# Performance work log

Hardware: AMD Instinct MI355X
Metric: run time of the kernel (lower is better)

Reference implementation:

```python
import jax, jax.numpy as jnp
import numpy as np


def _reduce1(x):
    # x: [B, n, d] -> [B, 2d]; exists=max, forall=min over objects (exclude_self is a no-op for cnt=1)
    return jnp.concatenate([x.max(axis=1), x.min(axis=1)], axis=-1)


def _reduce2(x):
    # x: [B, n, n, d] -> [B, n, 2d]; exclude_self masks diagonal i==j (0 for exists/max, 1 for forall/min)
    n = x.shape[1]
    diag = jnp.eye(n, dtype=bool)[None, :, :, None]
    exists = jnp.where(diag, 0.0, x).max(axis=2)
    forall = jnp.where(diag, 1.0, x).min(axis=2)
    return jnp.concatenate([exists, forall], axis=-1)


def _layer(f0, f1, f2, p):
    # One LogicLayer step (breadth=2, minmax reducer, exclude_self, sigmoid norm, no hidden layers)
    W0, b0, W1, b1, W2, b2 = p
    B, n, d1 = f1.shape
    # order 0: [self, reduce(order1)]
    g0 = jnp.concatenate([f0, _reduce1(f1)], axis=-1)
    o0 = jax.nn.sigmoid(g0 @ W0 + b0)
    # order 1: [expand(order0), self, reduce(order2)]
    e0 = jnp.broadcast_to(f0[:, None, :], (B, n, f0.shape[-1]))
    g1 = jnp.concatenate([e0, f1, _reduce2(f2)], axis=-1)
    o1 = jax.nn.sigmoid(g1 @ W1 + b1)
    # order 2: [expand(order1), self] then Permutation(2) = cat(x, swap(i,j))
    e1 = jnp.broadcast_to(f1[:, :, None, :], (B, n, n, d1))
    g2 = jnp.concatenate([e1, f2], axis=-1)
    g2 = jnp.concatenate([g2, jnp.swapaxes(g2, 1, 2)], axis=-1)
    o2 = jax.nn.sigmoid(g2 @ W2 + b2)
    return o0, o1, o2


def setup_inputs() -> dict:
    key = jax.random.key(0)
    B, n = 4, 256
    d = [32, 64, 64]
    O = 128
    ks = iter(jax.random.split(key, 64))
    inp = {
        "x0": jax.random.uniform(next(ks), (B, d[0]), dtype=jnp.float32),
        "x1": jax.random.uniform(next(ks), (B, n, d[1]), dtype=jnp.float32),
        "x2": jax.random.uniform(next(ks), (B, n, n, d[2]), dtype=jnp.float32),
    }
    fan_ins = [
        (d[0] + 2 * d[1], d[0] + d[1] + 2 * d[2], 2 * (d[1] + d[2])),  # layer 0
        (O + 2 * O, O + O + 2 * O, 2 * (O + O)),                        # layer 1
        (O + 2 * O, O + O + 2 * O, 2 * (O + O)),                        # layer 2
    ]
    for l, fins in enumerate(fan_ins):
        for o, fin in enumerate(fins):
            inp[f"W{o}_{l}"] = jax.random.normal(next(ks), (fin, O), dtype=jnp.float32) / np.sqrt(fin).astype(np.float32)
            inp[f"b{o}_{l}"] = jnp.zeros((O,), dtype=jnp.float32)
    return inp


def reference(x0, x1, x2,
              W0_0, b0_0, W1_0, b1_0, W2_0, b2_0,
              W0_1, b0_1, W1_1, b1_1, W2_1, b2_1,
              W0_2, b0_2, W1_2, b1_2, W2_2, b2_2):
    f = (x0, x1, x2)
    for p in ((W0_0, b0_0, W1_0, b1_0, W2_0, b2_0),
              (W0_1, b0_1, W1_1, b1_1, W2_1, b2_1),
              (W0_2, b0_2, W1_2, b1_2, W2_2, b2_2)):
        f = _layer(*f, p)
    return f
```

## Files before the change

### kernel.cpp

```cpp
#include <hip/hip_runtime.h>
#include <hip/hip_bf16.h>
#include <cstdint>

#define NN 256
#define NB 4
#define OC 128

using bf16x8_t = __attribute__((ext_vector_type(8))) __bf16;
using f32x4_t  = __attribute__((ext_vector_type(4))) float;

typedef const __attribute__((address_space(1))) uint8_t* gptr1_t;
typedef __attribute__((address_space(3))) uint8_t* lptr3_t;

__device__ __forceinline__ void async_load16(const void* g, void* l) {
  __builtin_amdgcn_global_load_lds((gptr1_t)g, (lptr3_t)l, 16, 0, 0);
}

__device__ __forceinline__ float sigf(float x) {
  return 1.0f / (1.0f + __expf(-x));
}

__device__ __forceinline__ uint16_t f2bf_rne(float f) {
  uint32_t u = __float_as_uint(f);
  uint32_t r = (u + 0x7fffu + ((u >> 16) & 1u)) >> 16;
  return (uint16_t)r;
}

__device__ __forceinline__ void emit_wt(const float* __restrict__ W2,
                                        uint16_t* __restrict__ Wt, int d1,
                                        int d2, int idx) {
  const int K = 2 * d2;
  const int nn = idx / K, k = idx - nn * K;
  const int row = (k < d2) ? (d1 + k) : (2 * d1 + d2 + (k - d2));
  Wt[idx] = f2bf_rne(W2[row * OC + nn]);
}

__device__ __forceinline__ void emit_bt(const float* __restrict__ W1,
                                        const float* __restrict__ W2, uint16_t* __restrict__ Bt,
                                        int D0, int D1, int D2, int FIN1,
                                        int KP, int idx) {
  const int n = idx / KP, k = idx - n * KP;
  float val = 0.f;
  if (n < 128) {
    if (k < FIN1) val = W1[k * OC + n];
  } else if (n < 256) {
    if (k >= D0 && k < D0 + D1) val = W2[(k - D0) * OC + (n - 128)];
  } else {
    if (k >= D0 && k < D0 + D1) val = W2[(D1 + D2 + (k - D0)) * OC + (n - 256)];
  }
  Bt[idx] = f2bf_rne(val);
}

__global__ __launch_bounds__(256) void prep_all(
    const float* __restrict__ W2_0, const float* __restrict__ W2_1,
    const float* __restrict__ W2_2, const float* __restrict__ W1_0,
    const float* __restrict__ W1_1, const float* __restrict__ W1_2,
    const float* __restrict__ x0, const float* __restrict__ x1,
    uint16_t* __restrict__ Wt0, uint16_t* __restrict__ Wt1,
    uint16_t* __restrict__ Wt2, uint16_t* __restrict__ Bt0,
    uint16_t* __restrict__ Bt1, uint16_t* __restrict__ Bt2,
    uint16_t* __restrict__ g1bf0, float* __restrict__ r2b,
    float* __restrict__ r2c, unsigned* __restrict__ cnt) {
  int g = blockIdx.x * 256 + threadIdx.x;
  if (g < 16384) { emit_wt(W2_0, Wt0, 64, 64, g); return; }
  g -= 16384;
  if (g < 32768) { emit_wt(W2_1, Wt1, 128, 128, g); return; }
  g -= 32768;
  if (g < 32768) { emit_wt(W2_2, Wt2, 128, 128, g); return; }
  g -= 32768;
  if (g < 98304) { emit_bt(W1_0, W2_0, Bt0, 32, 64, 64, 224, 256, g); return; }
  g -= 98304;
  if (g < 196608) { emit_bt(W1_1, W2_1, Bt1, 128, 128, 128, 512, 512, g); return; }
  g -= 196608;
  if (g < 196608) { emit_bt(W1_2, W2_2, Bt2, 128, 128, 128, 512, 512, g); return; }
  g -= 196608;
  if (g < 131072) {
    const int row = g >> 7, t = g & 127;
    uint16_t* const gp = g1bf0 + (size_t)row * 256;
    if (t < 32) gp[t] = f2bf_rne(x0[(row >> 8) * 32 + t]);
    else if (t < 96) gp[t] = f2bf_rne(x1[(size_t)row * 64 + (t - 32)]);
    else gp[128 + t] = 0;
    return;
  }
  g -= 131072;
  if (g < 262144) { r2b[g] = ((g & 255) < 128) ? 0.f : 1.f; return; }
  g -= 262144;
  if (g < 262144) { r2c[g] = ((g & 255) < 128) ? 0.f : 1.f; return; }
  g -= 262144;
  if (g < 2048) cnt[g] = 0u;
}

__global__ __launch_bounds__(256) void reduce2_l0_kernel(
    const float* __restrict__ x2, uint16_t* __restrict__ g1bf0,
    uint16_t* __restrict__ x2bf) {
  const int bid = blockIdx.x;
  const int i = bid & 255;
  const int tid = threadIdx.x;
  const int q = tid & 15, s = tid >> 4;
  const size_t rowbase = ((size_t)bid * NN) * 64 + q * 4;
  float mxA0 = 0.f, mxA1 = 0.f, mxA2 = 0.f, mxA3 = 0.f;
  float mnA0 = 1.f, mnA1 = 1.f, mnA2 = 1.f, mnA3 = 1.f;
  float mxB0 = 0.f, mxB1 = 0.f, mxB2 = 0.f, mxB3 = 0.f;
  float mnB0 = 1.f, mnB1 = 1.f, mnB2 = 1.f, mnB3 = 1.f;
#pragma unroll 2
  for (int t = 0; t < 16; t += 2) {
    const int jA = s + t * 16, jB = jA + 16;
    const float4 xa = *(const float4*)(x2 + rowbase + (size_t)jA * 64);
    const float4 xb = *(const float4*)(x2 + rowbase + (size_t)jB * 64);
    uint2 pa, pb;
    pa.x = (uint32_t)f2bf_rne(xa.x) | ((uint32_t)f2bf_rne(xa.y) << 16);
    pa.y = (uint32_t)f2bf_rne(xa.z) | ((uint32_t)f2bf_rne(xa.w) << 16);
    pb.x = (uint32_t)f2bf_rne(xb.x) | ((uint32_t)f2bf_rne(xb.y) << 16);
    pb.y = (uint32_t)f2bf_rne(xb.z) | ((uint32_t)f2bf_rne(xb.w) << 16);
    *(uint2*)(x2bf + rowbase + (size_t)jA * 64) = pa;
    *(uint2*)(x2bf + rowbase + (size_t)jB * 64) = pb;
    if (jA != i) {
      mxA0 = fmaxf(mxA0, xa.x); mxA1 = fmaxf(mxA1, xa.y);
      mxA2 = fmaxf(mxA2, xa.z); mxA3 = fmaxf(mxA3, xa.w);
      mnA0 = fminf(mnA0, xa.x); mnA1 = fminf(mnA1, xa.y);
      mnA2 = fminf(mnA2, xa.z); mnA3 = fminf(mnA3, xa.w);
    }
    if (jB != i) {
      mxB0 = fmaxf(mxB0, xb.x); mxB1 = fmaxf(mxB1, xb.y);
      mxB2 = fmaxf(mxB2, xb.z); mxB3 = fmaxf(mxB3, xb.w);
      mnB0 = fminf(mnB0, xb.x); mnB1 = fminf(mnB1, xb.y);
      mnB2 = fminf(mnB2, xb.z); mnB3 = fminf(mnB3, xb.w);
    }
  }
  float mx0 = fmaxf(mxA0, mxB0), mx1 = fmaxf(mxA1, mxB1);
  float mx2 = fmaxf(mxA2, mxB2), mx3 = fmaxf(mxA3, mxB3);
  float mn0 = fminf(mnA0, mnB0), mn1 = fminf(mnA1, mnB1);
  float mn2 = fminf(mnA2, mnB2), mn3 = fminf(mnA3, mnB3);
  __shared__ float4 smx[256], smn[256];
  smx[tid] = make_float4(mx0, mx1, mx2, mx3);
  smn[tid] = make_float4(mn0, mn1, mn2, mn3);
  __syncthreads();
  if (s == 0) {
    for (int ss = 1; ss < 16; ++ss) {
      float4 a = smx[q + ss * 16], c = smn[q + ss * 16];
      mx0 = fmaxf(mx0, a.x); mx1 = fmaxf(mx1, a.y);
      mx2 = fmaxf(mx2, a.z); mx3 = fmaxf(mx3, a.w);
      mn0 = fminf(mn0, c.x); mn1 = fminf(mn1, c.y);
      mn2 = fminf(mn2, c.z); mn3 = fminf(mn3, c.w);
    }
    uint16_t* const g = g1bf0 + (size_t)bid * 256;
    g[96 + q * 4 + 0] = f2bf_rne(mx0); g[96 + q * 4 + 1] = f2bf_rne(mx1);
    g[96 + q * 4 + 2] = f2bf_rne(mx2); g[96 + q * 4 + 3] = f2bf_rne(mx3);
    g[160 + q * 4 + 0] = f2bf_rne(mn0); g[160 + q * 4 + 1] = f2bf_rne(mn1);
    g[160 + q * 4 + 2] = f2bf_rne(mn2); g[160 + q * 4 + 3] = f2bf_rne(mn3);
  }
}

template <int KP, int D0, int D1, bool DUP>
__global__ __launch_bounds__(256) void small_gemm(
    const uint16_t* __restrict__ g1, const uint16_t* __restrict__ Bt,
    const float* __restrict__ b1, const float* __restrict__ b2,
    float* __restrict__ f1out, uint16_t* __restrict__ g1next,
    float* __restrict__ u, float* __restrict__ v,
    const float* __restrict__ f0in, const float* __restrict__ f1in,
    const float* __restrict__ W0, const float* __restrict__ b0,
    float* __restrict__ f0out) {
  constexpr int NCH = KP / 64;
  const int bid = blockIdx.x;
  const int tid = threadIdx.x;

  __shared__ __align__(16) uint8_t ldsA[8192];
  __shared__ __align__(16) uint8_t ldsB[16384];

  if (bid < 48) {
    const int mt = bid / 3, nt = bid - mt * 3;
    const int m0 = mt * 64, n0 = nt * 128;
    const int wv = tid >> 6, lane = tid & 63;
    const int l15 = lane & 15, l4 = lane >> 4;

    f32x4_t acc[4][2];
#pragma unroll
    for (int a = 0; a < 4; ++a)
#pragma unroll
      for (int q = 0; q < 2; ++q) acc[a][q] = (f32x4_t){0.f, 0.f, 0.f, 0.f};

    for (int c = 0; c < NCH; ++c) {
      const int kbg = c * 64;
#pragma unroll
      for (int t = 0; t < 2; ++t) {
        const int id = wv * 2 + t;
        const int mi = id & 3, ks = id >> 2;
        async_load16(g1 + (size_t)(m0 + mi * 16 + l15) * KP + kbg + ks * 32 + l4 * 8,
                     ldsA + id * 1024);
      }
#pragma unroll
      for (int t = 0; t < 4; ++t) {
        const int id = wv * 4 + t;
        const int ni = id & 7, ks = id >> 3;
        async_load16(Bt + (size_t)(n0 + ni * 16 + l15) * KP + kbg + ks * 32 + l4 * 8,
                     ldsB + id * 1024);
      }
      __syncthreads();
#pragma unroll
      for (int ks = 0; ks < 2; ++ks) {
        bf16x8_t Af[4], Bf[2];
#pragma unroll
        for (int a = 0; a < 4; ++a)
          Af[a] = *(const bf16x8_t*)(ldsA + ((ks * 4 + a) << 10) + (lane << 4));
#pragma unroll
        for (int q = 0; q < 2; ++q)
          Bf[q] = *(const bf16x8_t*)(ldsB + ((ks * 8 + wv * 2 + q) << 10) + (lane << 4));
#pragma unroll
        for (int a = 0; a < 4; ++a)
#pragma unroll
          for (int q = 0; q < 2; ++q)
            acc[a][q] = __builtin_amdgcn_mfma_f32_16x16x32_bf16(Af[a], Bf[q],
                                                                acc[a][q], 0, 0, 0);
      }
      __syncthreads();
    }

    float bias[2];
#pragma unroll
    for (int q = 0; q < 2; ++q) {
      const int cc = wv * 32 + q * 16 + l15;
      bias[q] = (nt == 0) ? b1[cc] : ((nt == 1) ? b2[cc] : 0.f);
    }
#pragma unroll
    for (int a = 0; a < 4; ++a) {
      const int rl = a * 16 + l4 * 4;
#pragma unroll
      for (int r = 0; r < 4; ++r) {
        const size_t bi = m0 + rl + r;
#pragma unroll
        for (int q = 0; q < 2; ++q) {
          const int cc = wv * 32 + q * 16 + l15;
          const float x = acc[a][q][r] + bias[q];
          if (nt == 0) {
            const float val = sigf(x);
            f1out[bi * OC + cc] = val;
            if (DUP) g1next[bi * 512 + 128 + cc] = f2bf_rne(val);
          } else if (nt == 1) {
            u[bi * OC + cc] = x;
          } else {
            v[bi * OC + cc] = x;
          }
        }
      }
    }
  } else {
    constexpr int FIN0 = D0 + 2 * D1;
    constexpr int S = 256 / D1;
    const int b = bid - 48;
    float* const sm = (float*)ldsA;
    float* const g0 = sm;
    float* const smx = sm + 512;
    float* const smn = sm + 768;
    float* const sval = sm + 1024;
    const int cc = tid & (D1 - 1), ss = tid / D1;
    float mx = -1e30f, mn = 1e30f;
    const float* f1b = f1in + (size_t)b * NN * D1;
    for (int j = ss; j < NN; j += S) {
      const float x = f1b[(size_t)j * D1 + cc];
      mx = fmaxf(mx, x); mn = fminf(mn, x);
    }
    smx[tid] = mx; smn[tid] = mn;
    __syncthreads();
    if (ss == 0) {
      for (int s2 = 1; s2 < S; ++s2) {
        mx = fmaxf(mx, smx[cc + s2 * D1]);
        mn = fminf(mn, smn[cc + s2 * D1]);
      }
      g0[D0 + cc] = mx;
      g0[D0 + D1 + cc] = mn;
    }
    if (tid < D0) g0[tid] = f0in[b * D0 + tid];
    __syncthreads();
    if (tid < OC) {
      float acc = b0[tid];
#pragma unroll 8
      for (int k = 0; k < FIN0; ++k) acc += g0[k] * W0[k * OC + tid];
      const float val = sigf(acc);
      f0out[b * OC + tid] = val;
      sval[tid] = val;
    }
    if (DUP) {
      __syncthreads();
      for (int idx = tid; idx < 256 * 128; idx += 256) {
        const int row = idx >> 7, c2 = idx & 127;
        g1next[((size_t)(b * 256 + row)) * 512 + c2] = f2bf_rne(sval[c2]);
      }
    }
  }
}

template <int D2, typename OUT_T, bool REDUCE>
__global__ __launch_bounds__(256, 3) void gemm2_kernel(
    const __hip_bfloat16* __restrict__ f2, const uint16_t* __restrict__ Wt,
    const float* __restrict__ u, const float* __restrict__ v,
    OUT_T* __restrict__ out, float* __restrict__ r2n,
    unsigned* __restrict__ cnt, uint16_t* __restrict__ g1next) {
  constexpr int K = 2 * D2;
  constexpr int NCH = K / 64;
  constexpr bool BF16OUT = (sizeof(OUT_T) == 2);
  constexpr int LDSB = BF16OUT ? (128 * 272) : 32768;
  const int bid = blockIdx.x;
  const int jt = bid & 1, i = (bid >> 1) & 255, b = bid >> 9;
  const int j0 = jt * 128;
  const int tid = threadIdx.x;
  const int wv = tid >> 6, lane = tid & 63;
  const int wr = wv >> 1, wc = wv & 1;
  const int l15 = lane & 15, l4 = lane >> 4;

  __shared__ __align__(16) uint8_t lds[LDSB];
  __shared__ unsigned smax[128], smin[128];
  __shared__ unsigned sflag;
  uint8_t* const ldsA = lds;
  uint8_t* const ldsW = lds + 16384;

  const __hip_bfloat16* A1 = f2 + ((size_t)(b * NN + i) * NN + j0) * D2;
  const __hip_bfloat16* A2 = f2 + ((size_t)(b * NN + j0) * NN + i) * D2;

  f32x4_t acc[4][4];
#pragma unroll
  for (int a = 0; a < 4; ++a)
#pragma unroll
    for (int q = 0; q < 4; ++q) acc[a][q] = (f32x4_t){0.f, 0.f, 0.f, 0.f};

  for (int c = 0; c < NCH; ++c) {
    const int kbg = c * 64;
    const bool second = (kbg >= D2);
    const __hip_bfloat16* Ab = second ? A2 : A1;
    const size_t rstride = second ? (size_t)NN * D2 : (size_t)D2;
    const int kbase = second ? (kbg - D2) : kbg;
#pragma unroll
    for (int q = 0; q < 4; ++q) {
      const int id = wv * 4 + q;
      const int mi = id & 7, ks = id >> 3;
      const int row = mi * 16 + l15;
      const int kk = ks * 32 + l4 * 8;
      async_load16(Ab + (size_t)row * rstride + kbase + kk, ldsA + id * 1024);
    }
#pragma unroll
    for (int q = 0; q < 4; ++q) {
      const int id = wv * 4 + q;
      const int ni = id & 7, ks = id >> 3;
      const int nn2 = ni * 16 + l15;
      const int kk = ks * 32 + l4 * 8;
      async_load16(Wt + (size_t)nn2 * K + kbg + kk, ldsW + id * 1024);
    }
    __syncthreads();
#pragma unroll
    for (int ks = 0; ks < 2; ++ks) {
      bf16x8_t Af[4], Bf[4];
#pragma unroll
      for (int a = 0; a < 4; ++a)
        Af[a] = *(const bf16x8_t*)(ldsA + ((ks * 8 + wr * 4 + a) << 10) + (lane << 4));
#pragma unroll
      for (int q = 0; q < 4; ++q)
        Bf[q] = *(const bf16x8_t*)(ldsW + ((ks * 8 + wc * 4 + q) << 10) + (lane << 4));
#pragma unroll
      for (int a = 0; a < 4; ++a)
#pragma unroll
        for (int q = 0; q < 4; ++q)
          acc[a][q] = __builtin_amdgcn_mfma_f32_16x16x32_bf16(Af[a], Bf[q],
                                                              acc[a][q], 0, 0, 0);
    }
    __syncthreads();
  }

  const size_t bi2 = (size_t)(b * NN + i);
  float uval[4];
#pragma unroll
  for (int q = 0; q < 4; ++q) uval[q] = u[bi2 * OC + wc * 64 + q * 16 + l15];
  const size_t obase = (bi2 * NN + j0) * OC;
  const size_t vbase = (size_t)(b * NN + j0) * OC;

  if (BF16OUT) {
    if (REDUCE && tid < 128) { smax[tid] = 0u; smin[tid] = 0x3f800000u; }
    __syncthreads();
    float lmx[4] = {0.f, 0.f, 0.f, 0.f};
    float lmn[4] = {1.f, 1.f, 1.f, 1.f};
#pragma unroll
    for (int a = 0; a < 4; ++a) {
      const int rowb = wr * 64 + a * 16 + l4 * 4;
#pragma unroll
      for (int r = 0; r < 4; ++r) {
        const int j = rowb + r;
        const bool excl = (j0 + j) == i;
#pragma unroll
        for (int q = 0; q < 4; ++q) {
          const int col = wc * 64 + q * 16 + l15;
          const float x = acc[a][q][r] + uval[q] + v[vbase + (size_t)j * OC + col];
          const float sg = sigf(x);
          *(uint16_t*)(lds + j * 272 + col * 2) = f2bf_rne(sg);
          if (REDUCE && !excl) {
            lmx[q] = fmaxf(lmx[q], sg);
            lmn[q] = fminf(lmn[q], sg);
          }
        }
      }
    }
    if (REDUCE) {
#pragma unroll
      for (int q = 0; q < 4; ++q) {
        const int col = wc * 64 + q * 16 + l15;
        atomicMax(&smax[col], __float_as_uint(lmx[q]));
        atomicMin(&smin[col], __float_as_uint(lmn[q]));
      }
    }
    __syncthreads();
    uint16_t* const outp = (uint16_t*)out;
#pragma unroll
    for (int ci = 0; ci < 8; ++ci) {
      const int chunk = ci * 256 + tid;
      const int row = chunk >> 4, off = chunk & 15;
      const uint4 val = *(const uint4*)(lds + row * 272 + off * 16);
      *(uint4*)(outp + obase + (size_t)row * OC + off * 8) = val;
    }
    if (REDUCE) {
      unsigned* const r2u = (unsigned*)r2n;
      if (tid < 128) {
        atomicMax(&r2u[bi2 * 256 + tid], smax[tid]);
        atomicMin(&r2u[bi2 * 256 + 128 + tid], smin[tid]);
      }
      __syncthreads();
      if (tid == 0) {
        __threadfence();
        sflag = (atomicAdd(&cnt[bi2], 1u) == 1u) ? 1u : 0u;
      }
      __syncthreads();
      if (sflag) {
        const unsigned uv2 = atomicOr(&r2u[bi2 * 256 + tid], 0u);
        g1next[bi2 * 512 + 256 + tid] = f2bf_rne(__uint_as_float(uv2));
      }
    }
  } else {
    float* const outp = (float*)out;
#pragma unroll
    for (int a = 0; a < 4; ++a) {
      const int rowb = wr * 64 + a * 16 + l4 * 4;
#pragma unroll
      for (int r = 0; r < 4; ++r) {
        const int j = rowb + r;
#pragma unroll
        for (int q = 0; q < 4; ++q) {
          const int col = wc * 64 + q * 16 + l15;
          const float x = acc[a][q][r] + uval[q] + v[vbase + (size_t)j * OC + col];
          outp[obase + (size_t)j * OC + col] = sigf(x);
        }
      }
    }
  }
}

extern "C" void kernel_launch(void* const* d_in, const int* in_sizes, int n_in,
                              void* d_out, int out_size, void* d_ws,
                              size_t ws_size, hipStream_t stream) {
  const float* x0 = (const float*)d_in[0];
  const float* x1 = (const float*)d_in[1];
  const float* x2 = (const float*)d_in[2];
  const float *Wp[3][3], *bp[3][3];
  for (int l = 0; l < 3; ++l)
    for (int o = 0; o < 3; ++o) {
      Wp[l][o] = (const float*)d_in[3 + l * 6 + o * 2];
      bp[l][o] = (const float*)d_in[3 + l * 6 + o * 2 + 1];
    }

  const size_t F2E = (size_t)NB * NN * NN * OC;
  const size_t X2E = (size_t)NB * NN * NN * 64;

  uint8_t* ws = (uint8_t*)d_ws;
  size_t off = 0;
  auto carve = [&](size_t bytes) -> uint8_t* {
    uint8_t* p = ws + off;
    off += (bytes + 255) & ~(size_t)255;
    return p;
  };
  float* f0a = (float*)carve((size_t)NB * OC * 4);
  float* f0b = (float*)carve((size_t)NB * OC * 4);
  float* f1a = (float*)carve((size_t)NB * NN * OC * 4);
  float* f1b = (float*)carve((size_t)NB * NN * OC * 4);
  float* r2b = (float*)carve((size_t)NB * NN * 256 * 4);
  float* r2c = (float*)carve((size_t)NB * NN * 256 * 4);
  float* uu  = (float*)carve((size_t)NB * NN * OC * 4);
  float* vv  = (float*)carve((size_t)NB * NN * OC * 4);
  unsigned* cnt = (unsigned*)carve((size_t)2 * NB * NN * 4);
  unsigned* cnt1 = cnt;
  unsigned* cnt2 = cnt + NB * NN;
  uint16_t* Wt0 = (uint16_t*)carve((size_t)OC * 128 * 2);
  uint16_t* Wt1 = (uint16_t*)carve((size_t)OC * 256 * 2);
  uint16_t* Wt2 = (uint16_t*)carve((size_t)OC * 256 * 2);
  uint16_t* Bt0 = (uint16_t*)carve((size_t)384 * 256 * 2);
  uint16_t* Bt1 = (uint16_t*)carve((size_t)384 * 512 * 2);
  uint16_t* Bt2 = (uint16_t*)carve((size_t)384 * 512 * 2);
  uint16_t* g1bf0 = (uint16_t*)carve((size_t)NB * NN * 256 * 2);
  uint16_t* g1bf1 = (uint16_t*)carve((size_t)NB * NN * 512 * 2);
  uint16_t* g1bf2 = (uint16_t*)carve((size_t)NB * NN * 512 * 2);
  __hip_bfloat16* f2a = (__hip_bfloat16*)carve(F2E * 2);

  __hip_bfloat16* f2b;
  uint16_t* x2bf;
  if (ws_size >= off + F2E * 2) {
    f2b = (__hip_bfloat16*)carve(F2E * 2);
    x2bf = (uint16_t*)f2b;
  } else {
    f2b = (__hip_bfloat16*)d_in[2];
    x2bf = (uint16_t*)carve(X2E * 2);
  }

  float* out_f0 = (float*)d_out;
  float* out_f1 = out_f0 + (size_t)NB * OC;
  float* out_f2 = out_f1 + (size_t)NB * NN * OC;

  prep_all<<<4808, 256, 0, stream>>>(Wp[0][2], Wp[1][2], Wp[2][2], Wp[0][1],
                                     Wp[1][1], Wp[2][1], x0, x1, Wt0, Wt1, Wt2,
                                     Bt0, Bt1, Bt2, g1bf0, r2b, r2c, cnt);
  reduce2_l0_kernel<<<NB * NN, 256, 0, stream>>>(x2, g1bf0, x2bf);

  small_gemm<256, 32, 64, true><<<52, 256, 0, stream>>>(
      g1bf0, Bt0, bp[0][1], bp[0][2], f1a, g1bf1, uu, vv, x0, x1, Wp[0][0],
      bp[0][0], f0a);
  gemm2_kernel<64, __hip_bfloat16, true><<<NB * NN * 2, 256, 0, stream>>>(
      (const __hip_bfloat16*)x2bf, Wt0, uu, vv, f2a, r2b, cnt1, g1bf1);

  small_gemm<512, 128, 128, true><<<52, 256, 0, stream>>>(
      g1bf1, Bt1, bp[1][1], bp[1][2], f1b, g1bf2, uu, vv, f0a, f1a, Wp[1][0],
      bp[1][0], f0b);
  gemm2_kernel<128, __hip_bfloat16, true><<<NB * NN * 2, 256, 0, stream>>>(
      f2a, Wt1, uu, vv, f2b, r2c, cnt2, g1bf2);

  small_gemm<512, 128, 128, false><<<52, 256, 0, stream>>>(
      g1bf2, Bt2, bp[2][1], bp[2][2], out_f1, nullptr, uu, vv, f0b, f1b,
      Wp[2][0], bp[2][0], out_f0);
  gemm2_kernel<128, float, false><<<NB * NN * 2, 256, 0, stream>>>(
      f2b, Wt2, uu, vv, out_f2, nullptr, nullptr, nullptr);
}
```

Measured before the change: 627.9 us.

## Transpose v buffer, replace last-block counter with separate r2 conversion kernel

The v projection is now stored transposed (b, col, j), so the gemm2 epilogue can read four consecutive j values per column with one float4 load instead of four scattered scalar loads. The atomic counter, threadfence and last-block flag used to convert the reduced r2 values to bf16 inside gemm2 are removed. A small conv_r2 kernel launched after each reducing gemm2 does that conversion instead. The gemm2 launch bound goes from 3 to 4 waves per SIMD, which may force register spills, and the two extra kernel launches add fixed overhead.

```diff
diff --git a/kernel.cpp b/kernel.cpp
--- a/kernel.cpp
+++ b/kernel.cpp
@@ -36,9 +36,10 @@
 }
 
 __device__ __forceinline__ void emit_bt(const float* __restrict__ W1,
-                                        const float* __restrict__ W2, uint16_t* __restrict__ Bt,
-                                        int D0, int D1, int D2, int FIN1,
-                                        int KP, int idx) {
+                                        const float* __restrict__ W2,
+                                        uint16_t* __restrict__ Bt, int D0,
+                                        int D1, int D2, int FIN1, int KP,
+                                        int idx) {
   const int n = idx / KP, k = idx - n * KP;
   float val = 0.f;
   if (n < 128) {
@@ -60,7 +61,7 @@
     uint16_t* __restrict__ Wt2, uint16_t* __restrict__ Bt0,
     uint16_t* __restrict__ Bt1, uint16_t* __restrict__ Bt2,
     uint16_t* __restrict__ g1bf0, float* __restrict__ r2b,
-    float* __restrict__ r2c, unsigned* __restrict__ cnt) {
+    float* __restrict__ r2c) {
   int g = blockIdx.x * 256 + threadIdx.x;
   if (g < 16384) { emit_wt(W2_0, Wt0, 64, 64, g); return; }
   g -= 16384;
@@ -85,9 +86,7 @@
   g -= 131072;
   if (g < 262144) { r2b[g] = ((g & 255) < 128) ? 0.f : 1.f; return; }
   g -= 262144;
-  if (g < 262144) { r2c[g] = ((g & 255) < 128) ? 0.f : 1.f; return; }
-  g -= 262144;
-  if (g < 2048) cnt[g] = 0u;
+  if (g < 262144) { r2c[g] = ((g & 255) < 128) ? 0.f : 1.f; }
 }
 
 __global__ __launch_bounds__(256) void reduce2_l0_kernel(
@@ -156,7 +155,7 @@
     const uint16_t* __restrict__ g1, const uint16_t* __restrict__ Bt,
     const float* __restrict__ b1, const float* __restrict__ b2,
     float* __restrict__ f1out, uint16_t* __restrict__ g1next,
-    float* __restrict__ u, float* __restrict__ v,
+    float* __restrict__ u, float* __restrict__ vT,
     const float* __restrict__ f0in, const float* __restrict__ f1in,
     const float* __restrict__ W0, const float* __restrict__ b0,
     float* __restrict__ f0out) {
@@ -238,7 +237,8 @@
           } else if (nt == 1) {
             u[bi * OC + cc] = x;
           } else {
-            v[bi * OC + cc] = x;
+            const int b = (int)(bi >> 8), j = (int)(bi & 255);
+            vT[((size_t)b * OC + cc) * NN + j] = x;
           }
         }
       }
@@ -289,12 +289,17 @@
   }
 }
 
+__global__ __launch_bounds__(256) void conv_r2_kernel(
+    const float* __restrict__ r2, uint16_t* __restrict__ g1next) {
+  const int bi = blockIdx.x, t = threadIdx.x;
+  g1next[(size_t)bi * 512 + 256 + t] = f2bf_rne(r2[(size_t)bi * 256 + t]);
+}
+
 template <int D2, typename OUT_T, bool REDUCE>
-__global__ __launch_bounds__(256, 3) void gemm2_kernel(
+__global__ __launch_bounds__(256, 4) void gemm2_kernel(
     const __hip_bfloat16* __restrict__ f2, const uint16_t* __restrict__ Wt,
-    const float* __restrict__ u, const float* __restrict__ v,
-    OUT_T* __restrict__ out, float* __restrict__ r2n,
-    unsigned* __restrict__ cnt, uint16_t* __restrict__ g1next) {
+    const float* __restrict__ u, const float* __restrict__ vT,
+    OUT_T* __restrict__ out, float* __restrict__ r2n) {
   constexpr int K = 2 * D2;
   constexpr int NCH = K / 64;
   constexpr bool BF16OUT = (sizeof(OUT_T) == 2);
@@ -309,7 +314,6 @@
 
   __shared__ __align__(16) uint8_t lds[LDSB];
   __shared__ unsigned smax[128], smin[128];
-  __shared__ unsigned sflag;
   uint8_t* const ldsA = lds;
   uint8_t* const ldsW = lds + 16384;
 
@@ -369,7 +373,7 @@
 #pragma unroll
   for (int q = 0; q < 4; ++q) uval[q] = u[bi2 * OC + wc * 64 + q * 16 + l15];
   const size_t obase = (bi2 * NN + j0) * OC;
-  const size_t vbase = (size_t)(b * NN + j0) * OC;
+  const float* const vTb = vT + (size_t)b * OC * NN;
 
   if (BF16OUT) {
     if (REDUCE && tid < 128) { smax[tid] = 0u; smin[tid] = 0x3f800000u; }
@@ -379,17 +383,18 @@
 #pragma unroll
     for (int a = 0; a < 4; ++a) {
       const int rowb = wr * 64 + a * 16 + l4 * 4;
-#pragma unroll
-      for (int r = 0; r < 4; ++r) {
-        const int j = rowb + r;
-        const bool excl = (j0 + j) == i;
-#pragma unroll
-        for (int q = 0; q < 4; ++q) {
-          const int col = wc * 64 + q * 16 + l15;
-          const float x = acc[a][q][r] + uval[q] + v[vbase + (size_t)j * OC + col];
+      const int jg = j0 + rowb;
+#pragma unroll
+      for (int q = 0; q < 4; ++q) {
+        const int col = wc * 64 + q * 16 + l15;
+        const float4 vq = *(const float4*)(vTb + (size_t)col * NN + jg);
+#pragma unroll
+        for (int r = 0; r < 4; ++r) {
+          const int j = rowb + r;
+          const float x = acc[a][q][r] + uval[q] + ((const float*)&vq)[r];
           const float sg = sigf(x);
           *(uint16_t*)(lds + j * 272 + col * 2) = f2bf_rne(sg);
-          if (REDUCE && !excl) {
+          if (REDUCE && (jg + r) != i) {
             lmx[q] = fmaxf(lmx[q], sg);
             lmn[q] = fminf(lmn[q], sg);
           }
@@ -413,35 +418,25 @@
       const uint4 val = *(const uint4*)(lds + row * 272 + off * 16);
       *(uint4*)(outp + obase + (size_t)row * OC + off * 8) = val;
     }
-    if (REDUCE) {
+    if (REDUCE && tid < 128) {
       unsigned* const r2u = (unsigned*)r2n;
-      if (tid < 128) {
-        atomicMax(&r2u[bi2 * 256 + tid], smax[tid]);
-        atomicMin(&r2u[bi2 * 256 + 128 + tid], smin[tid]);
-      }
-      __syncthreads();
-      if (tid == 0) {
-        __threadfence();
-        sflag = (atomicAdd(&cnt[bi2], 1u) == 1u) ? 1u : 0u;
-      }
-      __syncthreads();
-      if (sflag) {
-        const unsigned uv2 = atomicOr(&r2u[bi2 * 256 + tid], 0u);
-        g1next[bi2 * 512 + 256 + tid] = f2bf_rne(__uint_as_float(uv2));
-      }
+      atomicMax(&r2u[bi2 * 256 + tid], smax[tid]);
+      atomicMin(&r2u[bi2 * 256 + 128 + tid], smin[tid]);
     }
   } else {
     float* const outp = (float*)out;
 #pragma unroll
     for (int a = 0; a < 4; ++a) {
       const int rowb = wr * 64 + a * 16 + l4 * 4;
-#pragma unroll
-      for (int r = 0; r < 4; ++r) {
-        const int j = rowb + r;
-#pragma unroll
-        for (int q = 0; q < 4; ++q) {
-          const int col = wc * 64 + q * 16 + l15;
-          const float x = acc[a][q][r] + uval[q] + v[vbase + (size_t)j * OC + col];
+      const int jg = j0 + rowb;
+#pragma unroll
+      for (int q = 0; q < 4; ++q) {
+        const int col = wc * 64 + q * 16 + l15;
+        const float4 vq = *(const float4*)(vTb + (size_t)col * NN + jg);
+#pragma unroll
+        for (int r = 0; r < 4; ++r) {
+          const int j = rowb + r;
+          const float x = acc[a][q][r] + uval[q] + ((const float*)&vq)[r];
           outp[obase + (size_t)j * OC + col] = sigf(x);
         }
       }
@@ -479,10 +474,7 @@
   float* r2b = (float*)carve((size_t)NB * NN * 256 * 4);
   float* r2c = (float*)carve((size_t)NB * NN * 256 * 4);
   float* uu  = (float*)carve((size_t)NB * NN * OC * 4);
-  float* vv  = (float*)carve((size_t)NB * NN * OC * 4);
-  unsigned* cnt = (unsigned*)carve((size_t)2 * NB * NN * 4);
-  unsigned* cnt1 = cnt;
-  unsigned* cnt2 = cnt + NB * NN;
+  float* vT  = (float*)carve((size_t)NB * OC * NN * 4);
   uint16_t* Wt0 = (uint16_t*)carve((size_t)OC * 128 * 2);
   uint16_t* Wt1 = (uint16_t*)carve((size_t)OC * 256 * 2);
   uint16_t* Wt2 = (uint16_t*)carve((size_t)OC * 256 * 2);
@@ -508,26 +500,28 @@
   float* out_f1 = out_f0 + (size_t)NB * OC;
   float* out_f2 = out_f1 + (size_t)NB * NN * OC;
 
-  prep_all<<<4808, 256, 0, stream>>>(Wp[0][2], Wp[1][2], Wp[2][2], Wp[0][1],
+  prep_all<<<4800, 256, 0, stream>>>(Wp[0][2], Wp[1][2], Wp[2][2], Wp[0][1],
                                      Wp[1][1], Wp[2][1], x0, x1, Wt0, Wt1, Wt2,
-                                     Bt0, Bt1, Bt2, g1bf0, r2b, r2c, cnt);
+                                     Bt0, Bt1, Bt2, g1bf0, r2b, r2c);
   reduce2_l0_kernel<<<NB * NN, 256, 0, stream>>>(x2, g1bf0, x2bf);
 
   small_gemm<256, 32, 64, true><<<52, 256, 0, stream>>>(
-      g1bf0, Bt0, bp[0][1], bp[0][2], f1a, g1bf1, uu, vv, x0, x1, Wp[0][0],
+      g1bf0, Bt0, bp[0][1], bp[0][2], f1a, g1bf1, uu, vT, x0, x1, Wp[0][0],
       bp[0][0], f0a);
   gemm2_kernel<64, __hip_bfloat16, true><<<NB * NN * 2, 256, 0, stream>>>(
-      (const __hip_bfloat16*)x2bf, Wt0, uu, vv, f2a, r2b, cnt1, g1bf1);
+      (const __hip_bfloat16*)x2bf, Wt0, uu, vT, f2a, r2b);
+  conv_r2_kernel<<<NB * NN, 256, 0, stream>>>(r2b, g1bf1);
 
   small_gemm<512, 128, 128, true><<<52, 256, 0, stream>>>(
-      g1bf1, Bt1, bp[1][1], bp[1][2], f1b, g1bf2, uu, vv, f0a, f1a, Wp[1][0],
+      g1bf1, Bt1, bp[1][1], bp[1][2], f1b, g1bf2, uu, vT, f0a, f1a, Wp[1][0],
       bp[1][0], f0b);
   gemm2_kernel<128, __hip_bfloat16, true><<<NB * NN * 2, 256, 0, stream>>>(
-      f2a, Wt1, uu, vv, f2b, r2c, cnt2, g1bf2);
+      f2a, Wt1, uu, vT, f2b, r2c);
+  conv_r2_kernel<<<NB * NN, 256, 0, stream>>>(r2c, g1bf2);
 
   small_gemm<512, 128, 128, false><<<52, 256, 0, stream>>>(
-      g1bf2, Bt2, bp[2][1], bp[2][2], out_f1, nullptr, uu, vv, f0b, f1b,
+      g1bf2, Bt2, bp[2][1], bp[2][2], out_f1, nullptr, uu, vT, f0b, f1b,
       Wp[2][0], bp[2][0], out_f0);
   gemm2_kernel<128, float, false><<<NB * NN * 2, 256, 0, stream>>>(
-      f2b, Wt2, uu, vv, out_f2, nullptr, nullptr, nullptr);
-}
+      f2b, Wt2, uu, vT, out_f2, nullptr);
+}
```

Measured after the change: 518.7 us. 1.21x faster.
